# Performance work log

Hardware: AMD Instinct MI355X
Metric: run time of the kernel (lower is better)

## Reference

```python
import jax, jax.numpy as jnp
import numpy as np
import math

N_HEADS = 8
TANH_CLIP = 10.0
TEMP = 1.0


def setup_inputs() -> dict:
    key = jax.random.key(0)
    ks = jax.random.split(key, 8)
    B, N, D = 256, 2048, 128
    node_embeddings = jax.random.normal(ks[0], (B, N, D), dtype=jnp.float32)
    W_node = jax.random.normal(ks[1], (D, 3 * D), dtype=jnp.float32) / math.sqrt(D)
    W_fixed = jax.random.normal(ks[2], (D, D), dtype=jnp.float32) / math.sqrt(D)
    W_step = jax.random.normal(ks[3], (2 * D, D), dtype=jnp.float32) / math.sqrt(2 * D)
    W_out = jax.random.normal(ks[4], (D, D), dtype=jnp.float32) / math.sqrt(D)
    first_idx = jax.random.randint(ks[5], (B,), 0, N, dtype=jnp.int32)
    last_idx = jax.random.randint(ks[6], (B,), 0, N, dtype=jnp.int32)
    mask = jax.random.bernoulli(ks[7], 0.5, (B, N))
    mask = mask.at[:, 0].set(False)  # guarantee at least one feasible node per row
    return {"node_embeddings": node_embeddings, "W_node": W_node, "W_fixed": W_fixed,
            "W_step": W_step, "W_out": W_out, "first_idx": first_idx,
            "last_idx": last_idx, "mask": mask}


def reference(node_embeddings, W_node, W_fixed, W_step, W_out, first_idx, last_idx, mask):
    B, N, D = node_embeddings.shape
    H = N_HEADS
    hd = D // H  # key_dim = val_dim = embed_dim / n_heads
    neg_inf = -jnp.inf

    # --- _precompute ---
    graph_embed = node_embeddings.mean(axis=1)                # [B, D]
    fixed_context = graph_embed @ W_fixed                     # [B, D]
    proj = node_embeddings @ W_node                           # [B, N, 3D]
    gK, gV, logit_K = jnp.split(proj, 3, axis=-1)             # each [B, N, D]
    gK = gK.reshape(B, N, H, hd).transpose(2, 0, 1, 3)        # [H, B, N, hd]
    gV = gV.reshape(B, N, H, hd).transpose(2, 0, 1, 3)        # [H, B, N, hd]

    # --- step context: cat(first node emb, last node emb) ---
    first_emb = jnp.take_along_axis(node_embeddings, first_idx[:, None, None].astype(jnp.int32), axis=1)[:, 0]  # [B, D]
    last_emb = jnp.take_along_axis(node_embeddings, last_idx[:, None, None].astype(jnp.int32), axis=1)[:, 0]
    step_ctx = jnp.concatenate([first_emb, last_emb], axis=-1)  # [B, 2D]
    query = fixed_context + step_ctx @ W_step                 # [B, D]

    # --- glimpse multi-head attention (n_query = 1, masked inner) ---
    Q = query.reshape(B, H, hd).transpose(1, 0, 2)            # [H, B, hd]
    compat = jnp.einsum('hbd,hbnd->hbn', Q, gK) / math.sqrt(hd)  # [H, B, N]
    compat = jnp.where(mask[None, :, :], neg_inf, compat)     # mask_inner=True
    attn = jax.nn.softmax(compat, axis=-1)
    heads = jnp.einsum('hbn,hbnd->hbd', attn, gV)             # [H, B, hd]
    glimpse = heads.transpose(1, 0, 2).reshape(B, D) @ W_out  # project_out, [B, D]

    # --- logits with tanh clipping and masking ---
    logits = jnp.einsum('bd,bnd->bn', glimpse, logit_K) / math.sqrt(D)  # [B, N]
    logits = jnp.tanh(logits) * TANH_CLIP
    logits = jnp.where(mask, neg_inf, logits)                 # mask_logits=True
    log_p = jax.nn.log_softmax(logits / TEMP, axis=-1)        # [B, N]
    return log_p
```

## Files before the change

### kernel.cpp

```cpp
#include <hip/hip_runtime.h>
#include <math.h>

#define B_ 256
#define N_ 2048
#define D_ 128
#define GRID_F 512

#define NEG_HUGE (-1.0e30f)

#define WSQ_OFF 262144
#define WSA_OFF 524288
#define WSB_OFF_M 2654208
#define WSC_OFF_M 2658304
#define FLAGS_OFF 2691072
#define WS_NEED_BYTES ((size_t)(FLAGS_OFF + 1280) * 4)

#define WSA_STRIDE 1040
#define FB_WSB_OFF (B_ * 8 * WSA_STRIDE)
#define FB_WSC_OFF (FB_WSB_OFF + B_ * 8 * 2)

typedef __attribute__((ext_vector_type(8))) short bf16x8;
typedef __attribute__((ext_vector_type(4))) float f32x4;
typedef __attribute__((ext_vector_type(4))) unsigned short u16x4;
typedef __attribute__((ext_vector_type(2))) int i32x2;

__device__ __forceinline__ float wave_max64(float v) {
#pragma unroll
  for (int off = 32; off > 0; off >>= 1) v = fmaxf(v, __shfl_xor(v, off, 64));
  return v;
}
__device__ __forceinline__ float wave_sum64(float v) {
#pragma unroll
  for (int off = 32; off > 0; off >>= 1) v += __shfl_xor(v, off, 64);
  return v;
}
__device__ __forceinline__ unsigned short bf16rne(float f) {
  unsigned u = __float_as_uint(f);
  u += 0x7FFFu + ((u >> 16) & 1u);
  return (unsigned short)(u >> 16);
}
__device__ __forceinline__ float bflo(unsigned u) { return __uint_as_float(u << 16); }
__device__ __forceinline__ float bfhi(unsigned u) { return __uint_as_float(u & 0xFFFF0000u); }

__device__ __forceinline__ void do_D(const float* __restrict__ Wnode,
                                     const float* __restrict__ Wout,
                                     const float* __restrict__ wsA,
                                     float* __restrict__ wsC, int b, int t,
                                     unsigned char* smem) {
  float* Ls = (float*)smem;
  float* scale = Ls + 8;
  float* wl = scale + 64;
  float* heads = wl + 1024;
  float* glim = heads + 128;
  float* p2 = glim + 128;
  const int j = t & 127, hh = t >> 7;
  const float* base = wsA + (size_t)b * 8 * WSA_STRIDE;

  if (t < 8) {
    float M = -INFINITY;
#pragma unroll
    for (int s = 0; s < 8; ++s) M = fmaxf(M, base[s * WSA_STRIDE + t]);
    float L = 0.f;
#pragma unroll
    for (int s = 0; s < 8; ++s) {
      const float m = base[s * WSA_STRIDE + t];
      const float sc = (m == -INFINITY) ? 0.f : __expf(m - M);
      scale[s * 8 + t] = sc;
      L = fmaf(base[s * WSA_STRIDE + 8 + t], sc, L);
    }
    Ls[t] = L;
  }
  __syncthreads();
#pragma unroll
  for (int k = 0; k < 4; ++k) {
    const int idx = t + 256 * k;
    const int h = idx >> 7, d = idx & 127;
    float acc = 0.f;
#pragma unroll
    for (int s = 0; s < 8; ++s)
      acc = fmaf(scale[s * 8 + h], base[s * WSA_STRIDE + 16 + h * 128 + d], acc);
    wl[idx] = acc;
  }
  __syncthreads();
  {
    const int h = j >> 4, kk = j & 15;
    const float* wp = Wnode + 128 + h * 16 + kk;
    float acc = 0.f;
#pragma unroll 8
    for (int d = 64 * hh; d < 64 * hh + 64; ++d)
      acc = fmaf(wl[h * 128 + d], wp[(size_t)d * 384], acc);
    p2[hh * 128 + j] = acc;
  }
  __syncthreads();
  if (t < 128) heads[t] = (p2[t] + p2[128 + t]) / Ls[t >> 4];
  __syncthreads();
  {
    float acc = 0.f;
#pragma unroll 8
    for (int k = 64 * hh; k < 64 * hh + 64; ++k)
      acc = fmaf(heads[k], Wout[(size_t)k * 128 + j], acc);
    p2[hh * 128 + j] = acc;
  }
  __syncthreads();
  if (t < 128) glim[t] = p2[t] + p2[128 + t];
  __syncthreads();
  {
    const float* wr = Wnode + (size_t)j * 384 + 256;
    float acc = 0.f;
#pragma unroll 8
    for (int k = 64 * hh; k < 64 * hh + 64; ++k) acc = fmaf(wr[k], glim[k], acc);
    p2[hh * 128 + j] = acc;
  }
  __syncthreads();
  if (t < 128)
    wsC[(size_t)b * 128 + t] = (p2[t] + p2[128 + t]) * 0.08838834764831845f;
  __syncthreads();
}

__global__ void __launch_bounds__(256, 2) k_fused(
    const float* __restrict__ emb, const float* __restrict__ Wnode,
    const float* __restrict__ Wfix, const float* __restrict__ Wstep,
    const float* __restrict__ Wout, const int* __restrict__ fidx,
    const int* __restrict__ lidx, const unsigned char* __restrict__ mask,
    float* __restrict__ buf, float* __restrict__ wsF,
    unsigned* __restrict__ flg) {
  const int g = blockIdx.x, t = threadIdx.x;
  float* wsM = wsF;
  float* wsQ = wsF + WSQ_OFF;
  float* wsA = wsF + WSA_OFF;
  float* wsB = wsF + WSB_OFF_M;
  float* wsC = wsF + WSC_OFF_M;
  unsigned* aprog = flg;
  unsigned* qrdy = flg + 256;
  unsigned* cprog = flg + 512;
  unsigned* crdy = flg + 768;
  unsigned* eprog = flg + 1024;

  __shared__ __align__(16) unsigned short eSeg[36864];
  __shared__ __align__(16) unsigned char scratch[6464];
  __shared__ unsigned sh_old;

  const int lane = t & 63, w = t >> 6;
  const int lg = lane >> 4, lc = lane & 15;

#pragma unroll 1
  for (int pass = 0; pass < 4; ++pass) {
    const int seg = g + GRID_F * pass;
    const int b = seg >> 3, s = seg & 7;
    const float* src = emb + ((size_t)b * N_ + s * 256) * D_;
    const unsigned char* mrow = mask + (size_t)b * N_ + s * 256;

    {
      const int d0 = (t & 15) * 8;
      float p[8];
#pragma unroll
      for (int j = 0; j < 8; ++j) p[j] = 0.f;
#pragma unroll
      for (int i = 0; i < 16; ++i) {
        const int n = (t >> 4) + 16 * i;
        const float4 v0 = *(const float4*)(src + (size_t)n * D_ + d0);
        const float4 v1 = *(const float4*)(src + (size_t)n * D_ + d0 + 4);
        p[0] += v0.x; p[1] += v0.y; p[2] += v0.z; p[3] += v0.w;
        p[4] += v1.x; p[5] += v1.y; p[6] += v1.z; p[7] += v1.w;
        bf16x8 ev;
        ev[0] = (short)bf16rne(v0.x); ev[1] = (short)bf16rne(v0.y);
        ev[2] = (short)bf16rne(v0.z); ev[3] = (short)bf16rne(v0.w);
        ev[4] = (short)bf16rne(v1.x); ev[5] = (short)bf16rne(v1.y);
        ev[6] = (short)bf16rne(v1.z); ev[7] = (short)bf16rne(v1.w);
        const int widx = ((n >> 2) * 8 + (d0 >> 4)) * 72 + ((n & 3) << 4) + (d0 & 15);
        *(bf16x8*)&eSeg[widx] = ev;
      }
#pragma unroll
      for (int j = 0; j < 8; ++j) {
        p[j] += __shfl_xor(p[j], 16, 64);
        p[j] += __shfl_xor(p[j], 32, 64);
      }
      float* red = (float*)scratch;
      if (lane < 16) {
        float* dstp = red + w * 128 + lane * 8;
#pragma unroll
        for (int j = 0; j < 8; ++j) dstp[j] = p[j];
      }
      __syncthreads();
      if (t < 128)
        wsM[(size_t)(b * 8 + s) * 128 + t] =
            red[t] + red[128 + t] + red[256 + t] + red[384 + t];
      __syncthreads();
    }
    if (t == 0) { __threadfence(); sh_old = atomicAdd(&aprog[b], 1u); }
    __syncthreads();

    if (sh_old == 7u) {
      __threadfence();
      float* ge = (float*)scratch;
      float* fe = ge + 128;
      float* le = ge + 256;
      float* pq = ge + 384;
      float* q = ge + 640;
      if (t < 128) {
        float ssum = 0.f;
#pragma unroll
        for (int i = 0; i < 8; ++i) ssum += wsM[(size_t)(b * 8 + i) * 128 + t];
        ge[t] = ssum * (1.0f / 2048.0f);
        fe[t] = emb[((size_t)b * N_ + fidx[b]) * D_ + t];
        le[t] = emb[((size_t)b * N_ + lidx[b]) * D_ + t];
      }
      __syncthreads();
      {
        const int j = t & 127, h2 = t >> 7;
        float acc = 0.f;
#pragma unroll 4
        for (int k = 64 * h2; k < 64 * h2 + 64; ++k) {
          acc = fmaf(ge[k], Wfix[k * 128 + j], acc);
          acc = fmaf(fe[k], Wstep[k * 128 + j], acc);
          acc = fmaf(le[k], Wstep[(128 + k) * 128 + j], acc);
        }
        pq[h2 * 128 + j] = acc;
      }
      __syncthreads();
      if (t < 128) q[t] = pq[t] + pq[128 + t];
      __syncthreads();
      if (t < 128) {
        const float* wrow = Wnode + (size_t)t * 384;
#pragma unroll
        for (int h = 0; h < 8; ++h) {
          float a = 0.f;
#pragma unroll
          for (int k = 0; k < 16; ++k) a = fmaf(q[h * 16 + k], wrow[h * 16 + k], a);
          wsQ[(size_t)b * 1024 + h * 128 + t] = a * 0.25f;
        }
      }
      __syncthreads();
      if (t == 0) { __threadfence(); atomicExch(&qrdy[b], 1u); }
    }

    if (t == 0) {
      while (atomicAdd(&qrdy[b], 0u) == 0u) __builtin_amdgcn_s_sleep(8);
      __threadfence();
    }
    __syncthreads();
    {
      unsigned short* pT = (unsigned short*)scratch;
      float* red0 = (float*)(scratch + 2304);
      float* red1 = (float*)(scratch + 2560);
      float* resc = (float*)(scratch + 2816);

      bf16x8 bq[4];
#pragma unroll
      for (int ks = 0; ks < 4; ++ks)
#pragma unroll
        for (int j = 0; j < 8; ++j) bq[ks][j] = 0;
      if (lc < 8) {
        const float* qrow = wsQ + (size_t)b * 1024 + lc * 128;
#pragma unroll
        for (int ks = 0; ks < 4; ++ks)
#pragma unroll
          for (int j = 0; j < 8; ++j)
            bq[ks][j] = (short)bf16rne(qrow[32 * ks + 8 * lg + j]);
      }

      float m_run = -INFINITY, l_run = 0.f;
      f32x4 wacc0 = {0.f, 0.f, 0.f, 0.f}, wacc1 = {0.f, 0.f, 0.f, 0.f};

      for (int tile = 0; tile < 4; ++tile) {
        const unsigned short* eR = eSeg + tile * 9216;
        __syncthreads();

        f32x4 sAcc = {0.f, 0.f, 0.f, 0.f};
#pragma unroll
        for (int ks = 0; ks < 4; ++ks) {
          const int aidx = ((4 * w + (lc >> 2)) * 8 + 2 * ks + (lg >> 1)) * 72 +
                           ((lc & 3) << 4) + ((lg & 1) << 3);
          const bf16x8 af = *(const bf16x8*)&eR[aidx];
          sAcc = __builtin_amdgcn_mfma_f32_16x16x32_bf16(af, bq[ks], sAcc, 0, 0, 0);
        }

        float sv[4];
        bool mk[4];
        float tmax = -INFINITY;
#pragma unroll
        for (int r = 0; r < 4; ++r) {
          mk[r] = mrow[tile * 64 + 16 * w + 4 * lg + r] != 0;
          sv[r] = mk[r] ? -INFINITY : sAcc[r];
          tmax = fmaxf(tmax, sv[r]);
        }
        tmax = fmaxf(tmax, __shfl_xor(tmax, 16, 64));
        tmax = fmaxf(tmax, __shfl_xor(tmax, 32, 64));
        if (lane < 16) red0[w * 16 + lc] = tmax;
        __syncthreads();

        const float m_tile = fmaxf(fmaxf(red0[lc], red0[16 + lc]),
                                   fmaxf(red0[32 + lc], red0[48 + lc]));
        const float m_new = fmaxf(m_run, m_tile);
        const float rsc = (m_new == -INFINITY) ? 1.f : __expf(m_run - m_new);
        float psum = 0.f;
        unsigned short pu[4];
#pragma unroll
        for (int r = 0; r < 4; ++r) {
          const float p = mk[r] ? 0.f : __expf(sv[r] - m_new);
          psum += p;
          pu[r] = bf16rne(p);
        }
        m_run = m_new;
        psum += __shfl_xor(psum, 16, 64);
        psum += __shfl_xor(psum, 32, 64);
        if (lane < 16) red1[w * 16 + lc] = psum;
        *(u16x4*)&pT[lc * 72 + 16 * w + 4 * lg] = (u16x4){pu[0], pu[1], pu[2], pu[3]};
        if (t < 16) resc[t] = rsc;
        __syncthreads();

        l_run = l_run * rsc +
                (red1[lc] + red1[16 + lc] + red1[32 + lc] + red1[48 + lc]);
        {
          const float r0f = resc[4 * lg + 0], r1f = resc[4 * lg + 1];
          const float r2f = resc[4 * lg + 2], r3f = resc[4 * lg + 3];
          wacc0[0] *= r0f; wacc0[1] *= r1f; wacc0[2] *= r2f; wacc0[3] *= r3f;
          wacc1[0] *= r0f; wacc1[1] *= r1f; wacc1[2] *= r2f; wacc1[3] *= r3f;
        }

        i32x2 tb0a, tb0b, tb1a, tb1b, tb2a, tb2b, tb3a, tb3b;
        {
          const unsigned base00 = (unsigned)(unsigned long long)
              &eR[((0 + 2 * lg) * 8 + w) * 72 + lc];
          const unsigned base01 = (unsigned)(unsigned long long)
              &eR[((0 + 2 * lg) * 8 + (w + 4)) * 72 + lc];
          const unsigned base10 = (unsigned)(unsigned long long)
              &eR[((8 + 2 * lg) * 8 + w) * 72 + lc];
          const unsigned base11 = (unsigned)(unsigned long long)
              &eR[((8 + 2 * lg) * 8 + (w + 4)) * 72 + lc];
          asm volatile("ds_read_b64_tr_b16 %0, %2 offset:0\n\t"
                       "ds_read_b64_tr_b16 %1, %2 offset:1152"
                       : "=v"(tb0a), "=v"(tb0b) : "v"(base00));
          asm volatile("ds_read_b64_tr_b16 %0, %2 offset:0\n\t"
                       "ds_read_b64_tr_b16 %1, %2 offset:1152"
                       : "=v"(tb1a), "=v"(tb1b) : "v"(base01));
          asm volatile("ds_read_b64_tr_b16 %0, %2 offset:0\n\t"
                       "ds_read_b64_tr_b16 %1, %2 offset:1152"
                       : "=v"(tb2a), "=v"(tb2b) : "v"(base10));
          asm volatile("ds_read_b64_tr_b16 %0, %2 offset:0\n\t"
                       "ds_read_b64_tr_b16 %1, %2 offset:1152"
                       : "=v"(tb3a), "=v"(tb3b) : "v"(base11));
          asm volatile("s_waitcnt lgkmcnt(0)" ::: "memory");
          __builtin_amdgcn_sched_barrier(0);
        }
        {
          const bf16x8 pa0 = *(const bf16x8*)&pT[lc * 72 + 8 * lg];
          const bf16x8 pa1 = *(const bf16x8*)&pT[lc * 72 + 32 + 8 * lg];
          union { i32x2 d[2]; bf16x8 v; } u;
          u.d[0] = tb0a; u.d[1] = tb0b;
          wacc0 = __builtin_amdgcn_mfma_f32_16x16x32_bf16(pa0, u.v, wacc0, 0, 0, 0);
          u.d[0] = tb1a; u.d[1] = tb1b;
          wacc1 = __builtin_amdgcn_mfma_f32_16x16x32_bf16(pa0, u.v, wacc1, 0, 0, 0);
          u.d[0] = tb2a; u.d[1] = tb2b;
          wacc0 = __builtin_amdgcn_mfma_f32_16x16x32_bf16(pa1, u.v, wacc0, 0, 0, 0);
          u.d[0] = tb3a; u.d[1] = tb3b;
          wacc1 = __builtin_amdgcn_mfma_f32_16x16x32_bf16(pa1, u.v, wacc1, 0, 0, 0);
        }
      }
      __syncthreads();

      float* dst = wsA + (size_t)(b * 8 + s) * WSA_STRIDE;
      if (lg < 2) {
#pragma unroll
        for (int r = 0; r < 4; ++r) {
          const int h = 4 * lg + r;
          dst[16 + h * 128 + 16 * w + lc] = wacc0[r];
          dst[16 + h * 128 + 16 * (w + 4) + lc] = wacc1[r];
        }
      }
      if (t < 8) { dst[t] = m_run; dst[8 + t] = l_run; }
    }
    __syncthreads();
    if (t == 0) { __threadfence(); sh_old = atomicAdd(&cprog[b], 1u); }
    __syncthreads();

    if (sh_old == 7u) {
      __threadfence();
      do_D(Wnode, Wout, wsA, wsC, b, t, scratch);
      if (t == 0) { __threadfence(); atomicExch(&crdy[b], 1u); }
    }

    if (t == 0) {
      while (atomicAdd(&crdy[b], 0u) == 0u) __builtin_amdgcn_s_sleep(8);
      __threadfence();
    }
    __syncthreads();
    {
      float* lgs = (float*)scratch;
      const float4* c4 = (const float4*)(wsC + (size_t)b * 128);
      const float4 cfa = c4[(t & 15) * 2];
      const float4 cfb = c4[(t & 15) * 2 + 1];
      float mr = NEG_HUGE, sr = 0.f;
      for (int tile = 0; tile < 4; ++tile) {
        const int n0 = tile * 64;
#pragma unroll
        for (int i = 0; i < 4; ++i) {
          const int gid = t + 256 * i;
          const int r = gid >> 4, c8 = (gid & 15) * 8;
          const int nn = n0 + r;
          const int idx =
              ((nn >> 2) * 8 + (c8 >> 4)) * 72 + ((nn & 3) << 4) + (c8 & 15);
          const bf16x8 ev = *(const bf16x8*)&eSeg[idx];
          const uint4 u = *(const uint4*)&ev;
          float p = bflo(u.x) * cfa.x + bfhi(u.x) * cfa.y;
          p = fmaf(bflo(u.y), cfa.z, p); p = fmaf(bfhi(u.y), cfa.w, p);
          p = fmaf(bflo(u.z), cfb.x, p); p = fmaf(bfhi(u.z), cfb.y, p);
          p = fmaf(bflo(u.w), cfb.z, p); p = fmaf(bfhi(u.w), cfb.w, p);
          p += __shfl_xor(p, 8, 64);
          p += __shfl_xor(p, 4, 64);
          p += __shfl_xor(p, 2, 64);
          p += __shfl_xor(p, 1, 64);
          if ((t & 15) == 0) lgs[r] = p;
        }
        __syncthreads();
        const bool mk = mrow[n0 + lane] != 0;
        const float x = lgs[lane];
        const float ex = __expf(2.f * x);
        const float val = mk ? NEG_HUGE : (10.f - __fdividef(20.f, ex + 1.f));
        const float tm = wave_max64(val);
        const float mn = fmaxf(mr, tm);
        sr = sr * __expf(mr - mn) + wave_sum64(mk ? 0.f : __expf(val - mn));
        mr = mn;
        if (w == 0) buf[(size_t)b * N_ + s * 256 + n0 + lane] = val;
        __syncthreads();
      }
      if (t == 0) {
        wsB[(size_t)(b * 8 + s) * 2] = mr;
        wsB[(size_t)(b * 8 + s) * 2 + 1] = sr;
      }
    }
    __syncthreads();
    if (t == 0) { __threadfence(); sh_old = atomicAdd(&eprog[b], 1u); }
    __syncthreads();

    if (sh_old == 7u) {
      __threadfence();
      float M = NEG_HUGE;
#pragma unroll
      for (int q = 0; q < 8; ++q) M = fmaxf(M, wsB[(size_t)(b * 8 + q) * 2]);
      float S = 0.f;
#pragma unroll
      for (int q = 0; q < 8; ++q) {
        const float m = wsB[(size_t)(b * 8 + q) * 2];
        S += wsB[(size_t)(b * 8 + q) * 2 + 1] * __expf(m - M);
      }
      const float LS = M + logf(S);
#pragma unroll
      for (int i = 0; i < 8; ++i) {
        const size_t idx = (size_t)b * N_ + i * 256 + t;
        const float v = buf[idx];
        buf[idx] = (v <= -1.0e29f) ? NEG_HUGE : (v - LS);
      }
    }
    __syncthreads();
  }
}

__global__ void __launch_bounds__(256) k_prep(const float* __restrict__ emb,
                                              float* __restrict__ buf) {
  const int b = blockIdx.x, s = blockIdx.y, t = threadIdx.x;
  const int f4 = t & 31, g = t >> 5;
  const size_t rowbase = (size_t)b * N_;
  float4 acc = make_float4(0.f, 0.f, 0.f, 0.f);
  int n = s * 256 + g;
#pragma unroll 8
  for (int i = 0; i < 32; ++i, n += 8) {
    const float4 v = *(const float4*)(emb + (rowbase + n) * D_ + f4 * 4);
    acc.x += v.x; acc.y += v.y; acc.z += v.z; acc.w += v.w;
  }
  __shared__ float4 red[256];
  red[t] = acc;
  __syncthreads();
  if (g == 0) {
    float4 r = red[f4];
#pragma unroll
    for (int j = 1; j < 8; ++j) {
      const float4 a = red[j * 32 + f4];
      r.x += a.x; r.y += a.y; r.z += a.z; r.w += a.w;
    }
    *(float4*)(buf + (size_t)b * N_ + s * 128 + f4 * 4) = r;
  }
}

__global__ void __launch_bounds__(384) k_query(const float* __restrict__ emb,
                                               const float* __restrict__ Wfix,
                                               const float* __restrict__ Wstep,
                                               const float* __restrict__ Wnode,
                                               const int* __restrict__ fidx,
                                               const int* __restrict__ lidx,
                                               float* __restrict__ buf) {
  const int b = blockIdx.x, t = threadIdx.x;
  __shared__ float x[384];
  __shared__ float part[3][128];
  __shared__ float q[128];
  if (t < 128) {
    float ssum = 0.f;
#pragma unroll
    for (int i = 0; i < 8; ++i) ssum += buf[(size_t)b * N_ + i * 128 + t];
    x[t] = ssum * (1.0f / 2048.0f);
  } else if (t < 256) {
    x[t] = emb[((size_t)b * N_ + fidx[b]) * D_ + (t - 128)];
  } else {
    x[t] = emb[((size_t)b * N_ + lidx[b]) * D_ + (t - 256)];
  }
  __syncthreads();
  {
    const int seg = t >> 7, j = t & 127;
    const float* xs = &x[seg * 128];
    const float* Wp = (seg == 0) ? (Wfix + j) : (Wstep + (seg == 1 ? 0 : 128 * 128) + j);
    float acc = 0.f;
#pragma unroll 8
    for (int k = 0; k < 128; ++k) acc = fmaf(xs[k], Wp[(size_t)k * 128], acc);
    part[seg][j] = acc;
  }
  __syncthreads();
  if (t < 128) q[t] = part[0][t] + part[1][t] + part[2][t];
  __syncthreads();
  if (t < 128) {
    const float* wrow = Wnode + (size_t)t * 384;
#pragma unroll
    for (int h = 0; h < 8; ++h) {
      float a = 0.f;
#pragma unroll
      for (int k = 0; k < 16; ++k) a = fmaf(q[h * 16 + k], wrow[h * 16 + k], a);
      buf[(size_t)b * N_ + 1024 + h * 128 + t] = a * 0.25f;
    }
  }
}

__global__ void __launch_bounds__(256) k_attn_m(const float* __restrict__ emb,
                                                const unsigned char* __restrict__ mask,
                                                const float* __restrict__ buf,
                                                float* __restrict__ wsA) {
  const int b = blockIdx.x, s = blockIdx.y;
  const int t = threadIdx.x;
  const int lane = t & 63, w = t >> 6;
  const int lg = lane >> 4, lc = lane & 15;
  __shared__ __align__(16) unsigned short eR[9216];
  __shared__ __align__(16) unsigned short pT[16 * 72];
  __shared__ float red0[64];
  __shared__ float red1[64];
  __shared__ float resc[16];
  __shared__ unsigned char mask_s[64];
  bf16x8 bq[4];
#pragma unroll
  for (int ks = 0; ks < 4; ++ks)
#pragma unroll
    for (int j = 0; j < 8; ++j) bq[ks][j] = 0;
  if (lc < 8) {
    const float* qrow = buf + (size_t)b * N_ + 1024 + lc * 128;
#pragma unroll
    for (int ks = 0; ks < 4; ++ks)
#pragma unroll
      for (int j = 0; j < 8; ++j)
        bq[ks][j] = (short)bf16rne(qrow[32 * ks + 8 * lg + j]);
  }
  float m_run = -INFINITY, l_run = 0.f;
  f32x4 wacc0 = {0.f, 0.f, 0.f, 0.f}, wacc1 = {0.f, 0.f, 0.f, 0.f};
  const float* embb = emb + ((size_t)b * N_ + s * 256) * D_;
  const unsigned char* mrow = mask + (size_t)b * N_ + s * 256;
  for (int tile = 0; tile < 4; ++tile) {
    {
      const float* src = embb + (size_t)tile * 64 * D_;
#pragma unroll
      for (int i = 0; i < 4; ++i) {
        const int gid = t + 256 * i;
        const int n = gid >> 4, d0 = (gid & 15) * 8;
        const float4 v0 = *(const float4*)(src + (size_t)n * D_ + d0);
        const float4 v1 = *(const float4*)(src + (size_t)n * D_ + d0 + 4);
        bf16x8 ev;
        ev[0] = (short)bf16rne(v0.x); ev[1] = (short)bf16rne(v0.y);
        ev[2] = (short)bf16rne(v0.z); ev[3] = (short)bf16rne(v0.w);
        ev[4] = (short)bf16rne(v1.x); ev[5] = (short)bf16rne(v1.y);
        ev[6] = (short)bf16rne(v1.z); ev[7] = (short)bf16rne(v1.w);
        const int widx = ((n >> 2) * 8 + (d0 >> 4)) * 72 + ((n & 3) << 4) + (d0 & 15);
        *(bf16x8*)&eR[widx] = ev;
      }
      if (t < 64) mask_s[t] = mrow[tile * 64 + t];
    }
    __syncthreads();
    f32x4 sAcc = {0.f, 0.f, 0.f, 0.f};
#pragma unroll
    for (int ks = 0; ks < 4; ++ks) {
      const int aidx = ((4 * w + (lc >> 2)) * 8 + 2 * ks + (lg >> 1)) * 72 +
                       ((lc & 3) << 4) + ((lg & 1) << 3);
      const bf16x8 af = *(const bf16x8*)&eR[aidx];
      sAcc = __builtin_amdgcn_mfma_f32_16x16x32_bf16(af, bq[ks], sAcc, 0, 0, 0);
    }
    float sv[4];
    bool mk[4];
    float tmax = -INFINITY;
#pragma unroll
    for (int r = 0; r < 4; ++r) {
      mk[r] = mask_s[16 * w + 4 * lg + r] != 0;
      sv[r] = mk[r] ? -INFINITY : sAcc[r];
      tmax = fmaxf(tmax, sv[r]);
    }
    tmax = fmaxf(tmax, __shfl_xor(tmax, 16, 64));
    tmax = fmaxf(tmax, __shfl_xor(tmax, 32, 64));
    if (lane < 16) red0[w * 16 + lc] = tmax;
    __syncthreads();
    const float m_tile = fmaxf(fmaxf(red0[lc], red0[16 + lc]),
                               fmaxf(red0[32 + lc], red0[48 + lc]));
    const float m_new = fmaxf(m_run, m_tile);
    const float rsc = (m_new == -INFINITY) ? 1.f : __expf(m_run - m_new);
    float psum = 0.f;
    unsigned short pu[4];
#pragma unroll
    for (int r = 0; r < 4; ++r) {
      const float p = mk[r] ? 0.f : __expf(sv[r] - m_new);
      psum += p;
      pu[r] = bf16rne(p);
    }
    m_run = m_new;
    psum += __shfl_xor(psum, 16, 64);
    psum += __shfl_xor(psum, 32, 64);
    if (lane < 16) red1[w * 16 + lc] = psum;
    *(u16x4*)&pT[lc * 72 + 16 * w + 4 * lg] = (u16x4){pu[0], pu[1], pu[2], pu[3]};
    if (t < 16) resc[t] = rsc;
    __syncthreads();
    l_run = l_run * rsc + (red1[lc] + red1[16 + lc] + red1[32 + lc] + red1[48 + lc]);
    {
      const float r0f = resc[4 * lg + 0], r1f = resc[4 * lg + 1];
      const float r2f = resc[4 * lg + 2], r3f = resc[4 * lg + 3];
      wacc0[0] *= r0f; wacc0[1] *= r1f; wacc0[2] *= r2f; wacc0[3] *= r3f;
      wacc1[0] *= r0f; wacc1[1] *= r1f; wacc1[2] *= r2f; wacc1[3] *= r3f;
    }
    i32x2 tb0a, tb0b, tb1a, tb1b, tb2a, tb2b, tb3a, tb3b;
    {
      const unsigned base00 = (unsigned)(unsigned long long)
          &eR[((0 + 2 * lg) * 8 + w) * 72 + lc];
      const unsigned base01 = (unsigned)(unsigned long long)
          &eR[((0 + 2 * lg) * 8 + (w + 4)) * 72 + lc];
      const unsigned base10 = (unsigned)(unsigned long long)
          &eR[((8 + 2 * lg) * 8 + w) * 72 + lc];
      const unsigned base11 = (unsigned)(unsigned long long)
          &eR[((8 + 2 * lg) * 8 + (w + 4)) * 72 + lc];
      asm volatile("ds_read_b64_tr_b16 %0, %2 offset:0\n\t"
                   "ds_read_b64_tr_b16 %1, %2 offset:1152"
                   : "=v"(tb0a), "=v"(tb0b) : "v"(base00));
      asm volatile("ds_read_b64_tr_b16 %0, %2 offset:0\n\t"
                   "ds_read_b64_tr_b16 %1, %2 offset:1152"
                   : "=v"(tb1a), "=v"(tb1b) : "v"(base01));
      asm volatile("ds_read_b64_tr_b16 %0, %2 offset:0\n\t"
                   "ds_read_b64_tr_b16 %1, %2 offset:1152"
                   : "=v"(tb2a), "=v"(tb2b) : "v"(base10));
      asm volatile("ds_read_b64_tr_b16 %0, %2 offset:0\n\t"
                   "ds_read_b64_tr_b16 %1, %2 offset:1152"
                   : "=v"(tb3a), "=v"(tb3b) : "v"(base11));
      asm volatile("s_waitcnt lgkmcnt(0)" ::: "memory");
      __builtin_amdgcn_sched_barrier(0);
    }
    {
      const bf16x8 pa0 = *(const bf16x8*)&pT[lc * 72 + 8 * lg];
      const bf16x8 pa1 = *(const bf16x8*)&pT[lc * 72 + 32 + 8 * lg];
      union { i32x2 d[2]; bf16x8 v; } u;
      u.d[0] = tb0a; u.d[1] = tb0b;
      wacc0 = __builtin_amdgcn_mfma_f32_16x16x32_bf16(pa0, u.v, wacc0, 0, 0, 0);
      u.d[0] = tb1a; u.d[1] = tb1b;
      wacc1 = __builtin_amdgcn_mfma_f32_16x16x32_bf16(pa0, u.v, wacc1, 0, 0, 0);
      u.d[0] = tb2a; u.d[1] = tb2b;
      wacc0 = __builtin_amdgcn_mfma_f32_16x16x32_bf16(pa1, u.v, wacc0, 0, 0, 0);
      u.d[0] = tb3a; u.d[1] = tb3b;
      wacc1 = __builtin_amdgcn_mfma_f32_16x16x32_bf16(pa1, u.v, wacc1, 0, 0, 0);
    }
    __syncthreads();
  }
  float* dst = wsA + (size_t)(b * 8 + s) * WSA_STRIDE;
  if (lg < 2) {
#pragma unroll
    for (int r = 0; r < 4; ++r) {
      const int h = 4 * lg + r;
      dst[16 + h * 128 + 16 * w + lc] = wacc0[r];
      dst[16 + h * 128 + 16 * (w + 4) + lc] = wacc1[r];
    }
  }
  if (t < 8) { dst[t] = m_run; dst[8 + t] = l_run; }
}

__global__ void __launch_bounds__(256) k_attn_comb(const float* __restrict__ Wnode,
                                                   const float* __restrict__ Wout,
                                                   const float* __restrict__ wsA,
                                                   float* __restrict__ wsC) {
  __shared__ __align__(16) unsigned char smem[6464];
  do_D(Wnode, Wout, wsA, wsC, blockIdx.x, threadIdx.x, smem);
}

__global__ void __launch_bounds__(256) k_logits_part(const float* __restrict__ emb,
                                                     const unsigned char* __restrict__ mask,
                                                     const float* __restrict__ wsC,
                                                     float* __restrict__ buf,
                                                     float* __restrict__ wsB) {
  const int b = blockIdx.x, s = blockIdx.y;
  const int t = threadIdx.x, lane = t & 63, w = t >> 6;
  __shared__ float lg[64];
  const float4 cf = ((const float4*)(wsC + (size_t)b * 128))[t & 31];
  const float* embb = emb + ((size_t)b * N_ + s * 256) * D_;
  const unsigned char* mrow = mask + (size_t)b * N_ + s * 256;
  float mr = NEG_HUGE, sr = 0.f;
  for (int tile = 0; tile < 4; ++tile) {
    const int n0 = tile * 64;
#pragma unroll
    for (int i = 0; i < 8; ++i) {
      const int gid = t + 256 * i;
      const int r = gid >> 5, c = (gid & 31) * 4;
      const float4 e = *(const float4*)(embb + (size_t)(n0 + r) * D_ + c);
      float p = fmaf(e.x, cf.x, fmaf(e.y, cf.y, fmaf(e.z, cf.z, e.w * cf.w)));
      p += __shfl_xor(p, 16, 64);
      p += __shfl_xor(p, 8, 64);
      p += __shfl_xor(p, 4, 64);
      p += __shfl_xor(p, 2, 64);
      p += __shfl_xor(p, 1, 64);
      if ((t & 31) == 0) lg[r] = p;
    }
    __syncthreads();
    const bool mk = mrow[n0 + lane] != 0;
    const float x = lg[lane];
    const float ex = __expf(2.f * x);
    const float val = mk ? NEG_HUGE : (10.f - __fdividef(20.f, ex + 1.f));
    const float tm = wave_max64(val);
    const float mn = fmaxf(mr, tm);
    sr = sr * __expf(mr - mn) + wave_sum64(mk ? 0.f : __expf(val - mn));
    mr = mn;
    if (w == 0) buf[(size_t)b * N_ + s * 256 + n0 + lane] = val;
    __syncthreads();
  }
  if (t == 0) {
    wsB[(size_t)(b * 8 + s) * 2] = mr;
    wsB[(size_t)(b * 8 + s) * 2 + 1] = sr;
  }
}

__global__ void __launch_bounds__(256) k_norm(const float* __restrict__ wsB,
                                              float* __restrict__ buf) {
  const int b = blockIdx.x, s = blockIdx.y, t = threadIdx.x;
  float M = NEG_HUGE;
#pragma unroll
  for (int q = 0; q < 8; ++q) M = fmaxf(M, wsB[(size_t)(b * 8 + q) * 2]);
  float S = 0.f;
#pragma unroll
  for (int q = 0; q < 8; ++q) {
    const float m = wsB[(size_t)(b * 8 + q) * 2];
    S += wsB[(size_t)(b * 8 + q) * 2 + 1] * __expf(m - M);
  }
  const float LS = M + logf(S);
  const size_t idx = (size_t)b * N_ + s * 256 + t;
  const float v = buf[idx];
  buf[idx] = (v <= -1.0e29f) ? NEG_HUGE : (v - LS);
}

extern "C" void kernel_launch(void* const* d_in, const int* in_sizes, int n_in,
                              void* d_out, int out_size, void* d_ws, size_t ws_size,
                              hipStream_t stream) {
  (void)in_sizes; (void)n_in; (void)out_size;
  const float* emb = (const float*)d_in[0];
  const float* Wnode = (const float*)d_in[1];
  const float* Wfix = (const float*)d_in[2];
  const float* Wstep = (const float*)d_in[3];
  const float* Wout = (const float*)d_in[4];
  const int* fidx = (const int*)d_in[5];
  const int* lidx = (const int*)d_in[6];
  const unsigned char* mask = (const unsigned char*)d_in[7];
  float* buf = (float*)d_out;

  int occ = 0;
  (void)hipOccupancyMaxActiveBlocksPerMultiprocessor(&occ, k_fused, 256, 0);

  if (occ >= 2 && ws_size >= WS_NEED_BYTES) {
    float* wsF = (float*)d_ws;
    unsigned* flg = (unsigned*)(wsF + FLAGS_OFF);
    hipMemsetAsync(flg, 0, 1280 * 4, stream);
    k_fused<<<GRID_F, 256, 0, stream>>>(emb, Wnode, Wfix, Wstep, Wout, fidx,
                                        lidx, mask, buf, wsF, flg);
  } else {
    float* ws = (float*)d_ws;
    k_prep<<<dim3(B_, 8), 256, 0, stream>>>(emb, buf);
    k_query<<<B_, 384, 0, stream>>>(emb, Wfix, Wstep, Wnode, fidx, lidx, buf);
    k_attn_m<<<dim3(B_, 8), 256, 0, stream>>>(emb, mask, buf, ws);
    k_attn_comb<<<B_, 256, 0, stream>>>(Wnode, Wout, ws, ws + FB_WSC_OFF);
    k_logits_part<<<dim3(B_, 8), 256, 0, stream>>>(emb, mask, ws + FB_WSC_OFF, buf,
                                                   ws + FB_WSB_OFF);
    k_norm<<<dim3(B_, 8), 256, 0, stream>>>(ws + FB_WSB_OFF, buf);
  }
}
```

Measured before the change: 160.8 us.

## Split fused kernel into 128-node segments with 1024 persistent blocks

```diff
diff --git a/kernel.cpp b/kernel.cpp
--- a/kernel.cpp
+++ b/kernel.cpp
@@ -4,18 +4,19 @@
 #define B_ 256
 #define N_ 2048
 #define D_ 128
-#define GRID_F 512
+#define GRID_F 1024
 
 #define NEG_HUGE (-1.0e30f)
 
-#define WSQ_OFF 262144
-#define WSA_OFF 524288
-#define WSB_OFF_M 2654208
-#define WSC_OFF_M 2658304
-#define FLAGS_OFF 2691072
+#define WSM_OFF 0
+#define WSQ_OFF 524288
+#define WSA_OFF 786432
+#define WSB_OFF_M 5046272
+#define WSC_OFF_M 5054464
+#define FLAGS_OFF 5087232
 #define WS_NEED_BYTES ((size_t)(FLAGS_OFF + 1280) * 4)
-
 #define WSA_STRIDE 1040
+
 #define FB_WSB_OFF (B_ * 8 * WSA_STRIDE)
 #define FB_WSC_OFF (FB_WSB_OFF + B_ * 8 * 2)
 
@@ -42,82 +43,7 @@
 __device__ __forceinline__ float bflo(unsigned u) { return __uint_as_float(u << 16); }
 __device__ __forceinline__ float bfhi(unsigned u) { return __uint_as_float(u & 0xFFFF0000u); }
 
-__device__ __forceinline__ void do_D(const float* __restrict__ Wnode,
-                                     const float* __restrict__ Wout,
-                                     const float* __restrict__ wsA,
-                                     float* __restrict__ wsC, int b, int t,
-                                     unsigned char* smem) {
-  float* Ls = (float*)smem;
-  float* scale = Ls + 8;
-  float* wl = scale + 64;
-  float* heads = wl + 1024;
-  float* glim = heads + 128;
-  float* p2 = glim + 128;
-  const int j = t & 127, hh = t >> 7;
-  const float* base = wsA + (size_t)b * 8 * WSA_STRIDE;
-
-  if (t < 8) {
-    float M = -INFINITY;
-#pragma unroll
-    for (int s = 0; s < 8; ++s) M = fmaxf(M, base[s * WSA_STRIDE + t]);
-    float L = 0.f;
-#pragma unroll
-    for (int s = 0; s < 8; ++s) {
-      const float m = base[s * WSA_STRIDE + t];
-      const float sc = (m == -INFINITY) ? 0.f : __expf(m - M);
-      scale[s * 8 + t] = sc;
-      L = fmaf(base[s * WSA_STRIDE + 8 + t], sc, L);
-    }
-    Ls[t] = L;
-  }
-  __syncthreads();
-#pragma unroll
-  for (int k = 0; k < 4; ++k) {
-    const int idx = t + 256 * k;
-    const int h = idx >> 7, d = idx & 127;
-    float acc = 0.f;
-#pragma unroll
-    for (int s = 0; s < 8; ++s)
-      acc = fmaf(scale[s * 8 + h], base[s * WSA_STRIDE + 16 + h * 128 + d], acc);
-    wl[idx] = acc;
-  }
-  __syncthreads();
-  {
-    const int h = j >> 4, kk = j & 15;
-    const float* wp = Wnode + 128 + h * 16 + kk;
-    float acc = 0.f;
-#pragma unroll 8
-    for (int d = 64 * hh; d < 64 * hh + 64; ++d)
-      acc = fmaf(wl[h * 128 + d], wp[(size_t)d * 384], acc);
-    p2[hh * 128 + j] = acc;
-  }
-  __syncthreads();
-  if (t < 128) heads[t] = (p2[t] + p2[128 + t]) / Ls[t >> 4];
-  __syncthreads();
-  {
-    float acc = 0.f;
-#pragma unroll 8
-    for (int k = 64 * hh; k < 64 * hh + 64; ++k)
-      acc = fmaf(heads[k], Wout[(size_t)k * 128 + j], acc);
-    p2[hh * 128 + j] = acc;
-  }
-  __syncthreads();
-  if (t < 128) glim[t] = p2[t] + p2[128 + t];
-  __syncthreads();
-  {
-    const float* wr = Wnode + (size_t)j * 384 + 256;
-    float acc = 0.f;
-#pragma unroll 8
-    for (int k = 64 * hh; k < 64 * hh + 64; ++k) acc = fmaf(wr[k], glim[k], acc);
-    p2[hh * 128 + j] = acc;
-  }
-  __syncthreads();
-  if (t < 128)
-    wsC[(size_t)b * 128 + t] = (p2[t] + p2[128 + t]) * 0.08838834764831845f;
-  __syncthreads();
-}
-
-__global__ void __launch_bounds__(256, 2) k_fused(
+__global__ void __launch_bounds__(256, 4) k_fused(
     const float* __restrict__ emb, const float* __restrict__ Wnode,
     const float* __restrict__ Wfix, const float* __restrict__ Wstep,
     const float* __restrict__ Wout, const int* __restrict__ fidx,
@@ -125,7 +51,7 @@
     float* __restrict__ buf, float* __restrict__ wsF,
     unsigned* __restrict__ flg) {
   const int g = blockIdx.x, t = threadIdx.x;
-  float* wsM = wsF;
+  float* wsM = wsF + WSM_OFF;
   float* wsQ = wsF + WSQ_OFF;
   float* wsA = wsF + WSA_OFF;
   float* wsB = wsF + WSB_OFF_M;
@@ -136,8 +62,8 @@
   unsigned* crdy = flg + 768;
   unsigned* eprog = flg + 1024;
 
-  __shared__ __align__(16) unsigned short eSeg[36864];
-  __shared__ __align__(16) unsigned char scratch[6464];
+  __shared__ __align__(16) unsigned short eSeg[18432];
+  __shared__ __align__(16) unsigned char scratch[3840];
   __shared__ unsigned sh_old;
 
   const int lane = t & 63, w = t >> 6;
@@ -145,10 +71,13 @@
 
 #pragma unroll 1
   for (int pass = 0; pass < 4; ++pass) {
-    const int seg = g + GRID_F * pass;
-    const int b = seg >> 3, s = seg & 7;
-    const float* src = emb + ((size_t)b * N_ + s * 256) * D_;
-    const unsigned char* mrow = mask + (size_t)b * N_ + s * 256;
+    const int x = g & 7, y = g >> 3;
+    const int bp = x * 8 + (y >> 4);
+    const int m = y & 15;
+    const int b = pass * 64 + bp;
+    const int s = m;
+    const float* src = emb + ((size_t)b * N_ + s * 128) * D_;
+    const unsigned char* mrow = mask + (size_t)b * N_ + s * 128;
 
     {
       const int d0 = (t & 15) * 8;
@@ -156,7 +85,7 @@
 #pragma unroll
       for (int j = 0; j < 8; ++j) p[j] = 0.f;
 #pragma unroll
-      for (int i = 0; i < 16; ++i) {
+      for (int i = 0; i < 8; ++i) {
         const int n = (t >> 4) + 16 * i;
         const float4 v0 = *(const float4*)(src + (size_t)n * D_ + d0);
         const float4 v1 = *(const float4*)(src + (size_t)n * D_ + d0 + 4);
@@ -176,6 +105,7 @@
         p[j] += __shfl_xor(p[j], 32, 64);
       }
       float* red = (float*)scratch;
+      __syncthreads();
       if (lane < 16) {
         float* dstp = red + w * 128 + lane * 8;
 #pragma unroll
@@ -183,14 +113,14 @@
       }
       __syncthreads();
       if (t < 128)
-        wsM[(size_t)(b * 8 + s) * 128 + t] =
+        wsM[(size_t)(b * 16 + s) * 128 + t] =
             red[t] + red[128 + t] + red[256 + t] + red[384 + t];
       __syncthreads();
     }
     if (t == 0) { __threadfence(); sh_old = atomicAdd(&aprog[b], 1u); }
     __syncthreads();
 
-    if (sh_old == 7u) {
+    if (sh_old == 15u) {
       __threadfence();
       float* ge = (float*)scratch;
       float* fe = ge + 128;
@@ -200,7 +130,7 @@
       if (t < 128) {
         float ssum = 0.f;
 #pragma unroll
-        for (int i = 0; i < 8; ++i) ssum += wsM[(size_t)(b * 8 + i) * 128 + t];
+        for (int i = 0; i < 16; ++i) ssum += wsM[(size_t)(b * 16 + i) * 128 + t];
         ge[t] = ssum * (1.0f / 2048.0f);
         fe[t] = emb[((size_t)b * N_ + fidx[b]) * D_ + t];
         le[t] = emb[((size_t)b * N_ + lidx[b]) * D_ + t];
@@ -262,16 +192,16 @@
       float m_run = -INFINITY, l_run = 0.f;
       f32x4 wacc0 = {0.f, 0.f, 0.f, 0.f}, wacc1 = {0.f, 0.f, 0.f, 0.f};
 
-      for (int tile = 0; tile < 4; ++tile) {
-        const unsigned short* eR = eSeg + tile * 9216;
+      for (int tile = 0; tile < 2; ++tile) {
         __syncthreads();
 
         f32x4 sAcc = {0.f, 0.f, 0.f, 0.f};
 #pragma unroll
         for (int ks = 0; ks < 4; ++ks) {
-          const int aidx = ((4 * w + (lc >> 2)) * 8 + 2 * ks + (lg >> 1)) * 72 +
+          const int nsub = tile * 16 + 4 * w + (lc >> 2);
+          const int aidx = (nsub * 8 + 2 * ks + (lg >> 1)) * 72 +
                            ((lc & 3) << 4) + ((lg & 1) << 3);
-          const bf16x8 af = *(const bf16x8*)&eR[aidx];
+          const bf16x8 af = *(const bf16x8*)&eSeg[aidx];
           sAcc = __builtin_amdgcn_mfma_f32_16x16x32_bf16(af, bq[ks], sAcc, 0, 0, 0);
         }
 
@@ -321,13 +251,13 @@
         i32x2 tb0a, tb0b, tb1a, tb1b, tb2a, tb2b, tb3a, tb3b;
         {
           const unsigned base00 = (unsigned)(unsigned long long)
-              &eR[((0 + 2 * lg) * 8 + w) * 72 + lc];
+              &eSeg[((tile * 16 + 0 + 2 * lg) * 8 + w) * 72 + lc];
           const unsigned base01 = (unsigned)(unsigned long long)
-              &eR[((0 + 2 * lg) * 8 + (w + 4)) * 72 + lc];
+              &eSeg[((tile * 16 + 0 + 2 * lg) * 8 + (w + 4)) * 72 + lc];
           const unsigned base10 = (unsigned)(unsigned long long)
-              &eR[((8 + 2 * lg) * 8 + w) * 72 + lc];
+              &eSeg[((tile * 16 + 8 + 2 * lg) * 8 + w) * 72 + lc];
           const unsigned base11 = (unsigned)(unsigned long long)
-              &eR[((8 + 2 * lg) * 8 + (w + 4)) * 72 + lc];
+              &eSeg[((tile * 16 + 8 + 2 * lg) * 8 + (w + 4)) * 72 + lc];
           asm volatile("ds_read_b64_tr_b16 %0, %2 offset:0\n\t"
                        "ds_read_b64_tr_b16 %1, %2 offset:1152"
                        : "=v"(tb0a), "=v"(tb0b) : "v"(base00));
@@ -359,7 +289,7 @@
       }
       __syncthreads();
 
-      float* dst = wsA + (size_t)(b * 8 + s) * WSA_STRIDE;
+      float* dst = wsA + (size_t)(b * 16 + s) * WSA_STRIDE;
       if (lg < 2) {
 #pragma unroll
         for (int r = 0; r < 4; ++r) {
@@ -374,9 +304,80 @@
     if (t == 0) { __threadfence(); sh_old = atomicAdd(&cprog[b], 1u); }
     __syncthreads();
 
-    if (sh_old == 7u) {
+    if (sh_old == 15u) {
       __threadfence();
-      do_D(Wnode, Wout, wsA, wsC, b, t, scratch);
+      float* Ls = (float*)scratch;
+      float* scale = Ls + 8;
+      float* hv = scale + 128;
+      float* wlh = hv + 128;
+      const float* base = wsA + (size_t)b * 16 * WSA_STRIDE;
+
+      if (t < 8) {
+        float M = -INFINITY;
+#pragma unroll
+        for (int q = 0; q < 16; ++q) M = fmaxf(M, base[q * WSA_STRIDE + t]);
+        float L = 0.f;
+#pragma unroll
+        for (int q = 0; q < 16; ++q) {
+          const float mm = base[q * WSA_STRIDE + t];
+          const float sc = (mm == -INFINITY) ? 0.f : __expf(mm - M);
+          scale[q * 8 + t] = sc;
+          L = fmaf(base[q * WSA_STRIDE + 8 + t], sc, L);
+        }
+        Ls[t] = L;
+      }
+      __syncthreads();
+
+#pragma unroll
+      for (int half = 0; half < 2; ++half) {
+#pragma unroll
+        for (int k = 0; k < 2; ++k) {
+          const int idx = t + 256 * k;
+          const int hl = idx >> 7, d = idx & 127;
+          const int h = 4 * half + hl;
+          float acc = 0.f;
+#pragma unroll
+          for (int q = 0; q < 16; ++q)
+            acc = fmaf(scale[q * 8 + h], base[q * WSA_STRIDE + 16 + h * 128 + d], acc);
+          wlh[idx] = acc;
+        }
+        __syncthreads();
+        if (t < 64) {
+          const int j = 64 * half + t;
+          const int h = j >> 4, kk = j & 15;
+          const int hl = h - 4 * half;
+          const float* wp = Wnode + 128 + h * 16 + kk;
+          float acc = 0.f;
+          for (int d = 0; d < 128; ++d)
+            acc = fmaf(wlh[hl * 128 + d], wp[(size_t)d * 384], acc);
+          hv[j] = acc / Ls[h];
+        }
+        __syncthreads();
+      }
+
+      {
+        const int j = t & 127, hh = t >> 7;
+        float acc = 0.f;
+#pragma unroll 8
+        for (int k = 64 * hh; k < 64 * hh + 64; ++k)
+          acc = fmaf(hv[k], Wout[(size_t)k * 128 + j], acc);
+        wlh[hh * 128 + j] = acc;
+      }
+      __syncthreads();
+      if (t < 128) hv[t] = wlh[t] + wlh[128 + t];
+      __syncthreads();
+      {
+        const int j = t & 127, hh = t >> 7;
+        const float* wr = Wnode + (size_t)j * 384 + 256;
+        float acc = 0.f;
+#pragma unroll 8
+        for (int k = 64 * hh; k < 64 * hh + 64; ++k) acc = fmaf(wr[k], hv[k], acc);
+        wlh[hh * 128 + j] = acc;
+      }
+      __syncthreads();
+      if (t < 128)
+        wsC[(size_t)b * 128 + t] = (wlh[t] + wlh[128 + t]) * 0.08838834764831845f;
+      __syncthreads();
       if (t == 0) { __threadfence(); atomicExch(&crdy[b], 1u); }
     }
 
@@ -391,7 +392,7 @@
       const float4 cfa = c4[(t & 15) * 2];
       const float4 cfb = c4[(t & 15) * 2 + 1];
       float mr = NEG_HUGE, sr = 0.f;
-      for (int tile = 0; tile < 4; ++tile) {
+      for (int tile = 0; tile < 2; ++tile) {
         const int n0 = tile * 64;
 #pragma unroll
         for (int i = 0; i < 4; ++i) {
@@ -414,35 +415,35 @@
         }
         __syncthreads();
         const bool mk = mrow[n0 + lane] != 0;
-        const float x = lgs[lane];
-        const float ex = __expf(2.f * x);
+        const float xx = lgs[lane];
+        const float ex = __expf(2.f * xx);
         const float val = mk ? NEG_HUGE : (10.f - __fdividef(20.f, ex + 1.f));
         const float tm = wave_max64(val);
         const float mn = fmaxf(mr, tm);
         sr = sr * __expf(mr - mn) + wave_sum64(mk ? 0.f : __expf(val - mn));
         mr = mn;
-        if (w == 0) buf[(size_t)b * N_ + s * 256 + n0 + lane] = val;
+        if (w == 0) buf[(size_t)b * N_ + s * 128 + n0 + lane] = val;
         __syncthreads();
       }
       if (t == 0) {
-        wsB[(size_t)(b * 8 + s) * 2] = mr;
-        wsB[(size_t)(b * 8 + s) * 2 + 1] = sr;
+        wsB[(size_t)(b * 16 + s) * 2] = mr;
+        wsB[(size_t)(b * 16 + s) * 2 + 1] = sr;
       }
     }
     __syncthreads();
     if (t == 0) { __threadfence(); sh_old = atomicAdd(&eprog[b], 1u); }
     __syncthreads();
 
-    if (sh_old == 7u) {
+    if (sh_old == 15u) {
       __threadfence();
       float M = NEG_HUGE;
 #pragma unroll
-      for (int q = 0; q < 8; ++q) M = fmaxf(M, wsB[(size_t)(b * 8 + q) * 2]);
+      for (int q = 0; q < 16; ++q) M = fmaxf(M, wsB[(size_t)(b * 16 + q) * 2]);
       float S = 0.f;
 #pragma unroll
-      for (int q = 0; q < 8; ++q) {
-        const float m = wsB[(size_t)(b * 8 + q) * 2];
-        S += wsB[(size_t)(b * 8 + q) * 2 + 1] * __expf(m - M);
+      for (int q = 0; q < 16; ++q) {
+        const float mm = wsB[(size_t)(b * 16 + q) * 2];
+        S += wsB[(size_t)(b * 16 + q) * 2 + 1] * __expf(mm - M);
       }
       const float LS = M + logf(S);
 #pragma unroll
@@ -454,6 +455,80 @@
     }
     __syncthreads();
   }
+}
+
+__device__ __forceinline__ void do_D8(const float* __restrict__ Wnode,
+                                      const float* __restrict__ Wout,
+                                      const float* __restrict__ wsA,
+                                      float* __restrict__ wsC, int b, int t,
+                                      unsigned char* smem) {
+  float* Ls = (float*)smem;
+  float* scale = Ls + 8;
+  float* wl = scale + 64;
+  float* heads = wl + 1024;
+  float* glim = heads + 128;
+  float* p2 = glim + 128;
+  const int j = t & 127, hh = t >> 7;
+  const float* base = wsA + (size_t)b * 8 * WSA_STRIDE;
+
+  if (t < 8) {
+    float M = -INFINITY;
+#pragma unroll
+    for (int s = 0; s < 8; ++s) M = fmaxf(M, base[s * WSA_STRIDE + t]);
+    float L = 0.f;
+#pragma unroll
+    for (int s = 0; s < 8; ++s) {
+      const float m = base[s * WSA_STRIDE + t];
+      const float sc = (m == -INFINITY) ? 0.f : __expf(m - M);
+      scale[s * 8 + t] = sc;
+      L = fmaf(base[s * WSA_STRIDE + 8 + t], sc, L);
+    }
+    Ls[t] = L;
+  }
+  __syncthreads();
+#pragma unroll
+  for (int k = 0; k < 4; ++k) {
+    const int idx = t + 256 * k;
+    const int h = idx >> 7, d = idx & 127;
+    float acc = 0.f;
+#pragma unroll
+    for (int s = 0; s < 8; ++s)
+      acc = fmaf(scale[s * 8 + h], base[s * WSA_STRIDE + 16 + h * 128 + d], acc);
+    wl[idx] = acc;
+  }
+  __syncthreads();
+  {
+    const int h = j >> 4, kk = j & 15;
+    const float* wp = Wnode + 128 + h * 16 + kk;
+    float acc = 0.f;
+#pragma unroll 8
+    for (int d = 64 * hh; d < 64 * hh + 64; ++d)
+      acc = fmaf(wl[h * 128 + d], wp[(size_t)d * 384], acc);
+    p2[hh * 128 + j] = acc;
+  }
+  __syncthreads();
+  if (t < 128) heads[t] = (p2[t] + p2[128 + t]) / Ls[t >> 4];
+  __syncthreads();
+  {
+    float acc = 0.f;
+#pragma unroll 8
+    for (int k = 64 * hh; k < 64 * hh + 64; ++k)
+      acc = fmaf(heads[k], Wout[(size_t)k * 128 + j], acc);
+    p2[hh * 128 + j] = acc;
+  }
+  __syncthreads();
+  if (t < 128) glim[t] = p2[t] + p2[128 + t];
+  __syncthreads();
+  {
+    const float* wr = Wnode + (size_t)j * 384 + 256;
+    float acc = 0.f;
+#pragma unroll 8
+    for (int k = 64 * hh; k < 64 * hh + 64; ++k) acc = fmaf(wr[k], glim[k], acc);
+    p2[hh * 128 + j] = acc;
+  }
+  __syncthreads();
+  if (t < 128)
+    wsC[(size_t)b * 128 + t] = (p2[t] + p2[128 + t]) * 0.08838834764831845f;
 }
 
 __global__ void __launch_bounds__(256) k_prep(const float* __restrict__ emb,
@@ -683,7 +758,7 @@
                                                    const float* __restrict__ wsA,
                                                    float* __restrict__ wsC) {
   __shared__ __align__(16) unsigned char smem[6464];
-  do_D(Wnode, Wout, wsA, wsC, blockIdx.x, threadIdx.x, smem);
+  do_D8(Wnode, Wout, wsA, wsC, blockIdx.x, threadIdx.x, smem);
 }
 
 __global__ void __launch_bounds__(256) k_logits_part(const float* __restrict__ emb,
@@ -766,7 +841,7 @@
   int occ = 0;
   (void)hipOccupancyMaxActiveBlocksPerMultiprocessor(&occ, k_fused, 256, 0);
 
-  if (occ >= 2 && ws_size >= WS_NEED_BYTES) {
+  if (occ >= 4 && ws_size >= WS_NEED_BYTES) {
     float* wsF = (float*)d_ws;
     unsigned* flg = (unsigned*)(wsF + FLAGS_OFF);
     hipMemsetAsync(flg, 0, 1280 * 4, stream);
```

New measurement: 161.7 us. No clear change (+0.6%).
